# Kernel tuning notes

Measured on AMD Instinct MI355X. Metric: run time of the kernel, lower is better.

## Reference

```python
import jax, jax.numpy as jnp
import numpy as np


def axisangle2mat(p):
    # p: [N, 6] = (rotation vector rx,ry,rz, translation tx,ty,tz) -> [N, 3, 4]
    v = p[:, :3]
    t = p[:, 3:]
    theta = jnp.sqrt(jnp.sum(v * v, axis=-1) + 1e-12)  # [N]
    k = v / theta[:, None]
    kx, ky, kz = k[:, 0], k[:, 1], k[:, 2]
    zero = jnp.zeros_like(kx)
    K = jnp.stack([
        jnp.stack([zero, -kz, ky], -1),
        jnp.stack([kz, zero, -kx], -1),
        jnp.stack([-ky, kx, zero], -1),
    ], -2)  # [N,3,3]
    I = jnp.eye(3, dtype=p.dtype)
    s = jnp.sin(theta)[:, None, None]
    c = (1.0 - jnp.cos(theta))[:, None, None]
    R = I + s * K + c * jnp.matmul(K, K)
    return jnp.concatenate([R, t[:, :, None]], axis=-1)  # [N,3,4]


def grid_sample_3d(vol, grid):
    # vol: [D,H,W]; grid: [...,3] with last dim (x,y,z) in [-1,1].
    # Replicates F.grid_sample(mode='bilinear', padding_mode='zeros', align_corners=False).
    D, H, W = vol.shape
    ix = ((grid[..., 0] + 1.0) * W - 1.0) * 0.5
    iy = ((grid[..., 1] + 1.0) * H - 1.0) * 0.5
    iz = ((grid[..., 2] + 1.0) * D - 1.0) * 0.5
    x0 = jnp.floor(ix); y0 = jnp.floor(iy); z0 = jnp.floor(iz)
    fx = ix - x0; fy = iy - y0; fz = iz - z0
    vol_flat = vol.reshape(-1)
    out = jnp.zeros(grid.shape[:-1], vol.dtype)
    for dz in (0, 1):
        for dy in (0, 1):
            for dx in (0, 1):
                xc = x0 + dx; yc = y0 + dy; zc = z0 + dz
                wgt = ((fx if dx else 1.0 - fx) * (fy if dy else 1.0 - fy) * (fz if dz else 1.0 - fz))
                valid = ((xc >= 0) & (xc < W) & (yc >= 0) & (yc < H) & (zc >= 0) & (zc < D))
                xi = jnp.clip(xc, 0, W - 1).astype(jnp.int32)
                yi = jnp.clip(yc, 0, H - 1).astype(jnp.int32)
                zi = jnp.clip(zc, 0, D - 1).astype(jnp.int32)
                v = vol_flat[(zi * H + yi) * W + xi]
                out = out + jnp.where(valid, v * wgt, 0.0)
    return out


def setup_inputs() -> dict:
    key = jax.random.key(0)
    ks = jax.random.split(key, 8)
    B, n, D, H, W = 4096, 2048, 256, 256, 256
    x = jax.random.normal(ks[0], (1, 1, D, H, W), dtype=jnp.float32)
    # voxel-space sample points inside the volume
    sampleGrid = jax.random.uniform(ks[1], (B, 3), dtype=jnp.float32) * jnp.array([W - 1, H - 1, D - 1], jnp.float32)
    ax = jnp.concatenate([
        jax.random.normal(ks[2], (B, 1, 3), dtype=jnp.float32) * 0.1,   # small rotations
        jax.random.normal(ks[3], (B, 1, 3), dtype=jnp.float32) * 5.0,   # translations (voxels)
    ], axis=-1)
    low = jax.random.uniform(ks[4], (B, 1, 3), dtype=jnp.float32) * 2.0
    ext = jax.random.uniform(ks[5], (B, 1, 3), dtype=jnp.float32) * 4.0 + 1.0
    bound = jnp.concatenate([low, low + ext], axis=1)  # [B,2,3], bound[:,1] > bound[:,0]
    A = jax.random.normal(ks[6], (B, 3, 3), dtype=jnp.float32) * 0.3
    InvCovScaled = jnp.einsum('bij,bkj->bik', A, A) + 0.5 * jnp.eye(3, dtype=jnp.float32)  # SPD
    xyz_psf = jax.random.normal(ks[7], (B, n, 3), dtype=jnp.float32)
    psf_sigma = jnp.ones((1,), jnp.float32)  # unused in forward (as in the original)
    return dict(x=x, sampleGrid=sampleGrid, ax=ax, bound=bound,
                InvCovScaled=InvCovScaled, psf_sigma=psf_sigma, xyz_psf=xyz_psf)


def reference(x, sampleGrid, ax, bound, InvCovScaled, psf_sigma, xyz_psf):
    # x: [1,1,D,H,W]; sampleGrid: [B,3]; ax: [B,1,6]; bound: [B,2,3];
    # InvCovScaled: [B,3,3]; xyz_psf: [B,n,3] (the torch.randn draw, made explicit)
    W = x.shape[-1]; H = x.shape[-2]; D = x.shape[-3]
    size = (W, H, D)  # matches torch: size = [x.shape[-1], x.shape[-2], x.shape[-3]]
    scaled_xyz_psf = 2.0 * jax.nn.sigmoid(xyz_psf) - 1.0                      # [B,n,3]
    half = (bound[:, 1, :] - bound[:, 0, :]) * 0.5                            # [B,3]
    bound_psf = scaled_xyz_psf * half[:, None]                                # [B,n,3]
    mat = axisangle2mat(ax.reshape(-1, 6)).reshape(ax.shape[:-1] + (3, 4))    # [B,1,3,4]
    R = mat[:, 0, :, :3]                                                      # [B,3,3]
    T = mat[:, 0, :, 3]                                                       # [B,3]
    # trans_first=True: R @ (p + T)
    mat_sampleGrid = jnp.einsum('bij,bj->bi', R, sampleGrid + T)[:, None]     # [B,1,3]
    psf_sampleGrid = mat_sampleGrid + bound_psf                               # [B,n,3]
    norm = jnp.array([size[0] - 1, size[1] - 1, size[2] - 1], psf_sampleGrid.dtype)
    grid = 2.0 * (psf_sampleGrid / norm - 0.5)
    psf_x = grid_sample_3d(x[0, 0], grid)                                     # [B,n]
    # Mahalanobis-style weights: exp(-0.5 * c^T InvCov c)
    q = jnp.einsum('bni,bij,bnj->bn', bound_psf, InvCovScaled, bound_psf)
    w = jnp.exp(-0.5 * q)                                                     # [B,n]
    y = jnp.sum(psf_x * w, axis=-1) / jnp.sum(w, axis=-1)                     # [B]
    return y
```

## Files before the change

### kernel.cpp

```cpp
#include <hip/hip_runtime.h>
#include <math.h>

constexpr int NT   = 256;
constexpr int DIMV = 256;
constexpr int RS   = 8;
constexpr int RROW = 9;
constexpr int RSLICE = RS * RROW;

__global__ __launch_bounds__(NT) void psf_sample_kernel(
    const float* __restrict__ vol,
    const float* __restrict__ sampleGrid,
    const float* __restrict__ ax,
    const float* __restrict__ bound,
    const float* __restrict__ invcov,
    const float* __restrict__ xyz,
    float* __restrict__ out,
    int n)
{
    const int b   = blockIdx.x;
    const int tid = threadIdx.x;

    __shared__ float s_vol[RS * RSLICE];
    __shared__ float s_red[2 * (NT / 64)];

    const float v0 = ax[b*6+0], v1 = ax[b*6+1], v2 = ax[b*6+2];
    const float t0 = ax[b*6+3], t1 = ax[b*6+4], t2 = ax[b*6+5];
    const float theta = sqrtf(v0*v0 + v1*v1 + v2*v2 + 1e-12f);
    const float inv = 1.0f / theta;
    const float kx = v0*inv, ky = v1*inv, kz = v2*inv;
    const float sn = sinf(theta);
    const float cn = 1.0f - cosf(theta);
    const float R00 = 1.0f - cn*(ky*ky + kz*kz);
    const float R01 = -sn*kz + cn*kx*ky;
    const float R02 =  sn*ky + cn*kx*kz;
    const float R10 =  sn*kz + cn*kx*ky;
    const float R11 = 1.0f - cn*(kx*kx + kz*kz);
    const float R12 = -sn*kx + cn*ky*kz;
    const float R20 = -sn*ky + cn*kx*kz;
    const float R21 =  sn*kx + cn*ky*kz;
    const float R22 = 1.0f - cn*(kx*kx + ky*ky);
    const float g0 = sampleGrid[b*3+0] + t0;
    const float g1 = sampleGrid[b*3+1] + t1;
    const float g2 = sampleGrid[b*3+2] + t2;
    const float ms0 = R00*g0 + R01*g1 + R02*g2;
    const float ms1 = R10*g0 + R11*g1 + R12*g2;
    const float ms2 = R20*g0 + R21*g1 + R22*g2;
    const float h0 = (bound[b*6+3] - bound[b*6+0]) * 0.5f;
    const float h1 = (bound[b*6+4] - bound[b*6+1]) * 0.5f;
    const float h2 = (bound[b*6+5] - bound[b*6+2]) * 0.5f;
    const float M00 = invcov[b*9+0], M01 = invcov[b*9+1], M02 = invcov[b*9+2];
    const float M11 = invcov[b*9+4], M12 = invcov[b*9+5], M22 = invcov[b*9+8];

    const float kk = 256.0f / 255.0f;
    const float cix = ms0 * kk - 0.5f;
    const float ciy = ms1 * kk - 0.5f;
    const float ciz = ms2 * kk - 0.5f;
    const float hx = h0 * kk, hy = h1 * kk, hz = h2 * kk;

    const int bx = (int)floorf(cix - hx - 1e-3f);
    const int by = (int)floorf(ciy - hy - 1e-3f);
    const int bz = (int)floorf(ciz - hz - 1e-3f);
    const bool fast = (hx <= 2.9f) && (hy <= 2.9f) && (hz <= 2.9f);

    if (fast) {
        for (int idx = tid; idx < RS*RS*RS; idx += NT) {
            const int lx = idx & 7, ly = (idx >> 3) & 7, lz = idx >> 6;
            const int gx = bx + lx, gy = by + ly, gz = bz + lz;
            float v = 0.0f;
            if ((unsigned)gx < (unsigned)DIMV && (unsigned)gy < (unsigned)DIMV &&
                (unsigned)gz < (unsigned)DIMV)
                v = vol[((size_t)gz * DIMV + gy) * DIMV + gx];
            s_vol[(lz * RS + ly) * RROW + lx] = v;
        }
    }
    __syncthreads();

    float sum_wx = 0.0f, sum_w = 0.0f;
    const float* __restrict__ xb = xyz + (size_t)b * n * 3;

    for (int i = tid; i < n; i += NT) {
        const float rx = xb[i*3 + 0];
        const float ry = xb[i*3 + 1];
        const float rz = xb[i*3 + 2];
        const float ex = __expf(-rx), ey = __expf(-ry), ez = __expf(-rz);
        const float sx = (1.0f - ex) * __builtin_amdgcn_rcpf(1.0f + ex);
        const float sy = (1.0f - ey) * __builtin_amdgcn_rcpf(1.0f + ey);
        const float sz = (1.0f - ez) * __builtin_amdgcn_rcpf(1.0f + ez);
        const float bp0 = sx * h0, bp1 = sy * h1, bp2 = sz * h2;

        const float ixf = fmaf(bp0, kk, cix);
        const float iyf = fmaf(bp1, kk, ciy);
        const float izf = fmaf(bp2, kk, ciz);

        const float x0f = floorf(ixf), y0f = floorf(iyf), z0f = floorf(izf);
        const float fx = ixf - x0f, fy = iyf - y0f, fz = izf - z0f;

        float val;
        if (fast) {
            const int lx = min(max((int)x0f - bx, 0), RS - 2);
            const int ly = min(max((int)y0f - by, 0), RS - 2);
            const int lz = min(max((int)z0f - bz, 0), RS - 2);
            const float* p = &s_vol[(lz * RS + ly) * RROW + lx];
            const float v000 = p[0],              v001 = p[1];
            const float v010 = p[RROW],           v011 = p[RROW + 1];
            const float v100 = p[RSLICE],         v101 = p[RSLICE + 1];
            const float v110 = p[RSLICE + RROW],  v111 = p[RSLICE + RROW + 1];
            const float a00 = fmaf(fx, v001 - v000, v000);
            const float a01 = fmaf(fx, v011 - v010, v010);
            const float a10 = fmaf(fx, v101 - v100, v100);
            const float a11 = fmaf(fx, v111 - v110, v110);
            const float a0  = fmaf(fy, a01 - a00, a00);
            const float a1  = fmaf(fy, a11 - a10, a10);
            val = fmaf(fz, a1 - a0, a0);
        } else {
            const int x0 = (int)x0f, y0 = (int)y0f, z0 = (int)z0f;
            const int x1 = x0 + 1, y1 = y0 + 1, z1 = z0 + 1;
            const bool vx0 = (unsigned)x0 < (unsigned)DIMV;
            const bool vx1 = (unsigned)x1 < (unsigned)DIMV;
            const bool vy0 = (unsigned)y0 < (unsigned)DIMV;
            const bool vy1 = (unsigned)y1 < (unsigned)DIMV;
            const bool vz0 = (unsigned)z0 < (unsigned)DIMV;
            const bool vz1 = (unsigned)z1 < (unsigned)DIMV;
            const int cx0 = min(max(x0,0),DIMV-1), cx1 = min(max(x1,0),DIMV-1);
            const int cy0 = min(max(y0,0),DIMV-1), cy1 = min(max(y1,0),DIMV-1);
            const int cz0 = min(max(z0,0),DIMV-1), cz1 = min(max(z1,0),DIMV-1);
            const float wx0 = 1.0f-fx, wx1 = fx, wy0 = 1.0f-fy, wy1 = fy;
            const float wz0 = 1.0f-fz, wz1 = fz;
            const int r00 = (cz0*DIMV + cy0)*DIMV, r01 = (cz0*DIMV + cy1)*DIMV;
            const int r10 = (cz1*DIMV + cy0)*DIMV, r11 = (cz1*DIMV + cy1)*DIMV;
            val  = (vz0&&vy0&&vx0) ? vol[r00+cx0]*(wz0*wy0*wx0) : 0.0f;
            val += (vz0&&vy0&&vx1) ? vol[r00+cx1]*(wz0*wy0*wx1) : 0.0f;
            val += (vz0&&vy1&&vx0) ? vol[r01+cx0]*(wz0*wy1*wx0) : 0.0f;
            val += (vz0&&vy1&&vx1) ? vol[r01+cx1]*(wz0*wy1*wx1) : 0.0f;
            val += (vz1&&vy0&&vx0) ? vol[r10+cx0]*(wz1*wy0*wx0) : 0.0f;
            val += (vz1&&vy0&&vx1) ? vol[r10+cx1]*(wz1*wy0*wx1) : 0.0f;
            val += (vz1&&vy1&&vx0) ? vol[r11+cx0]*(wz1*wy1*wx0) : 0.0f;
            val += (vz1&&vy1&&vx1) ? vol[r11+cx1]*(wz1*wy1*wx1) : 0.0f;
        }

        const float q = M00*bp0*bp0 + M11*bp1*bp1 + M22*bp2*bp2
                      + 2.0f*(M01*bp0*bp1 + M02*bp0*bp2 + M12*bp1*bp2);
        const float w = __expf(-0.5f * q);
        sum_w  += w;
        sum_wx = fmaf(w, val, sum_wx);
    }

    #pragma unroll
    for (int off = 32; off > 0; off >>= 1) {
        sum_wx += __shfl_down(sum_wx, off);
        sum_w  += __shfl_down(sum_w,  off);
    }
    const int wave = tid >> 6;
    const int lane = tid & 63;
    if (lane == 0) { s_red[wave*2] = sum_wx; s_red[wave*2+1] = sum_w; }
    __syncthreads();
    if (tid == 0) {
        float twx = 0.0f, tw = 0.0f;
        #pragma unroll
        for (int wv = 0; wv < NT/64; ++wv) { twx += s_red[wv*2]; tw += s_red[wv*2+1]; }
        out[b] = twx / tw;
    }
}

extern "C" void kernel_launch(void* const* d_in, const int* in_sizes, int n_in,
                              void* d_out, int out_size, void* d_ws, size_t ws_size,
                              hipStream_t stream) {
    const float* vol        = (const float*)d_in[0];
    const float* sampleGrid = (const float*)d_in[1];
    const float* ax         = (const float*)d_in[2];
    const float* bound      = (const float*)d_in[3];
    const float* invcov     = (const float*)d_in[4];
    const float* xyz        = (const float*)d_in[6];
    float* out              = (float*)d_out;

    const int B = in_sizes[1] / 3;
    const int n = in_sizes[6] / (B * 3);

    psf_sample_kernel<<<B, NT, 0, stream>>>(vol, sampleGrid, ax, bound, invcov,
                                            xyz, out, n);
}
```

Baseline: 30.36 us.

## Vectorize xyz loads as float4 groups and fold Mahalanobis constants per block

```diff
diff --git a/kernel.cpp b/kernel.cpp
--- a/kernel.cpp
+++ b/kernel.cpp
@@ -51,6 +51,13 @@
     const float M00 = invcov[b*9+0], M01 = invcov[b*9+1], M02 = invcov[b*9+2];
     const float M11 = invcov[b*9+4], M12 = invcov[b*9+5], M22 = invcov[b*9+8];
 
+    const float B00 = -0.5f * M00 * h0 * h0;
+    const float B11 = -0.5f * M11 * h1 * h1;
+    const float B22 = -0.5f * M22 * h2 * h2;
+    const float B01 = -M01 * h0 * h1;
+    const float B02 = -M02 * h0 * h2;
+    const float B12 = -M12 * h1 * h2;
+
     const float kk = 256.0f / 255.0f;
     const float cix = ms0 * kk - 0.5f;
     const float ciy = ms1 * kk - 0.5f;
@@ -63,7 +70,9 @@
     const bool fast = (hx <= 2.9f) && (hy <= 2.9f) && (hz <= 2.9f);
 
     if (fast) {
-        for (int idx = tid; idx < RS*RS*RS; idx += NT) {
+        #pragma unroll
+        for (int pass = 0; pass < (RS*RS*RS)/NT; ++pass) {
+            const int idx = pass * NT + tid;
             const int lx = idx & 7, ly = (idx >> 3) & 7, lz = idx >> 6;
             const int gx = bx + lx, gy = by + ly, gz = bz + lz;
             float v = 0.0f;
@@ -76,30 +85,24 @@
     __syncthreads();
 
     float sum_wx = 0.0f, sum_w = 0.0f;
-    const float* __restrict__ xb = xyz + (size_t)b * n * 3;
-
-    for (int i = tid; i < n; i += NT) {
-        const float rx = xb[i*3 + 0];
-        const float ry = xb[i*3 + 1];
-        const float rz = xb[i*3 + 2];
+
+    auto doSample = [&](float rx, float ry, float rz) {
         const float ex = __expf(-rx), ey = __expf(-ry), ez = __expf(-rz);
         const float sx = (1.0f - ex) * __builtin_amdgcn_rcpf(1.0f + ex);
         const float sy = (1.0f - ey) * __builtin_amdgcn_rcpf(1.0f + ey);
         const float sz = (1.0f - ez) * __builtin_amdgcn_rcpf(1.0f + ez);
-        const float bp0 = sx * h0, bp1 = sy * h1, bp2 = sz * h2;
-
-        const float ixf = fmaf(bp0, kk, cix);
-        const float iyf = fmaf(bp1, kk, ciy);
-        const float izf = fmaf(bp2, kk, ciz);
-
+
+        const float ixf = fmaf(sx, hx, cix);
+        const float iyf = fmaf(sy, hy, ciy);
+        const float izf = fmaf(sz, hz, ciz);
         const float x0f = floorf(ixf), y0f = floorf(iyf), z0f = floorf(izf);
         const float fx = ixf - x0f, fy = iyf - y0f, fz = izf - z0f;
 
         float val;
         if (fast) {
-            const int lx = min(max((int)x0f - bx, 0), RS - 2);
-            const int ly = min(max((int)y0f - by, 0), RS - 2);
-            const int lz = min(max((int)z0f - bz, 0), RS - 2);
+            const int lx = (int)x0f - bx;
+            const int ly = (int)y0f - by;
+            const int lz = (int)z0f - bz;
             const float* p = &s_vol[(lz * RS + ly) * RROW + lx];
             const float v000 = p[0],              v001 = p[1];
             const float v010 = p[RROW],           v011 = p[RROW + 1];
@@ -138,12 +141,31 @@
             val += (vz1&&vy1&&vx1) ? vol[r11+cx1]*(wz1*wy1*wx1) : 0.0f;
         }
 
-        const float q = M00*bp0*bp0 + M11*bp1*bp1 + M22*bp2*bp2
-                      + 2.0f*(M01*bp0*bp1 + M02*bp0*bp2 + M12*bp1*bp2);
-        const float w = __expf(-0.5f * q);
+        const float f = fmaf(B00, sx*sx,
+                        fmaf(B11, sy*sy,
+                        fmaf(B22, sz*sz,
+                        fmaf(B01, sx*sy,
+                        fmaf(B02, sx*sz, B12 * (sy*sz))))));
+        const float w = __expf(f);
         sum_w  += w;
         sum_wx = fmaf(w, val, sum_wx);
-    }
+    };
+
+    const int ng = n >> 2;
+    const float4* __restrict__ xb4 =
+        reinterpret_cast<const float4*>(xyz + (size_t)b * n * 3);
+    for (int g = tid; g < ng; g += NT) {
+        const float4 q0 = xb4[g*3 + 0];
+        const float4 q1 = xb4[g*3 + 1];
+        const float4 q2 = xb4[g*3 + 2];
+        doSample(q0.x, q0.y, q0.z);
+        doSample(q0.w, q1.x, q1.y);
+        doSample(q1.z, q1.w, q2.x);
+        doSample(q2.y, q2.z, q2.w);
+    }
+    const float* __restrict__ xb = xyz + (size_t)b * n * 3;
+    for (int i = (ng << 2) + tid; i < n; i += NT)
+        doSample(xb[i*3+0], xb[i*3+1], xb[i*3+2]);
 
     #pragma unroll
     for (int off = 32; off > 0; off >>= 1) {
```

Result: no change. 30.02 us (-1.1%).
